# Kernel tuning notes

Hardware: AMD Instinct MI355X
Metric: run time of the kernel (lower is better)

Reference implementation:

```python
import jax, jax.numpy as jnp
import numpy as np

B, T, N, IN, H, K = 8, 10, 50, 6, 256, 4
E = N * (N - 1)


def setup_inputs() -> dict:
    key = jax.random.key(0)
    ks = jax.random.split(key, 22)
    p = lambda k, shape: jax.random.normal(k, shape, jnp.float32) * 0.05
    return {
        "inputs": jax.random.normal(ks[0], (B, T, N, IN), jnp.float32),
        "sampled_edges": jax.random.uniform(ks[1], (B, T, E, K), dtype=jnp.float32),
        "msg_w1": p(ks[2], (K, H, 2 * H)), "msg_b1": p(ks[3], (K, H)),
        "msg_w2": p(ks[4], (K, H, H)), "msg_b2": p(ks[5], (K, H)),
        "w_hr": p(ks[6], (H, H)), "w_hi": p(ks[7], (H, H)), "w_hh": p(ks[8], (H, H)),
        "w_ir": p(ks[9], (H, IN)), "b_ir": p(ks[10], (H,)),
        "w_ii": p(ks[11], (H, IN)), "b_ii": p(ks[12], (H,)),
        "w_in": p(ks[13], (H, IN)), "b_in": p(ks[14], (H,)),
        "w_o1": p(ks[15], (H, H)), "b_o1": p(ks[16], (H,)),
        "w_o2": p(ks[17], (H, H)), "b_o2": p(ks[18], (H,)),
        "w_o3": p(ks[19], (IN, H)), "b_o3": p(ks[20], (IN,)),
    }


def reference(inputs, sampled_edges, msg_w1, msg_b1, msg_w2, msg_b2,
              w_hr, w_hi, w_hh, w_ir, b_ir, w_ii, b_ii, w_in, b_in,
              w_o1, b_o1, w_o2, b_o2, w_o3, b_o3):
    b, t, n, _ = inputs.shape
    k = msg_w1.shape[0]
    h = msg_w1.shape[1]
    # fully-connected directed graph, no self loops (static indices)
    send_np, recv_np = np.where(np.ones((n, n)) - np.eye(n))
    send = jnp.asarray(send_np)
    recv = jnp.asarray(recv_np)
    norm = float(k) - 1.0  # skip_first_edge_type = True

    def single_step(ins, rel, hidden):
        # ins: [B,N,IN], rel: [B,E,K], hidden: [B,N,H]
        pre = jnp.concatenate([hidden[:, recv], hidden[:, send]], axis=-1)  # [B,E,2H]
        all_msgs = jnp.zeros((b, pre.shape[1], h), inputs.dtype)
        for i in range(1, k):  # skip first edge type
            m = jnp.tanh(jnp.einsum('bef,hf->beh', pre, msg_w1[i]) + msg_b1[i])
            m = jnp.tanh(jnp.einsum('beh,jh->bej', m, msg_w2[i]) + msg_b2[i])
            all_msgs = all_msgs + m * rel[:, :, i:i + 1] / norm
        # scatter-add messages to receiver nodes (replaces onehot matmul)
        agg = jnp.zeros((b, n, h), inputs.dtype).at[:, recv].add(all_msgs) / (n - 1)
        r = jax.nn.sigmoid(ins @ w_ir.T + b_ir + agg @ w_hr.T)
        ig = jax.nn.sigmoid(ins @ w_ii.T + b_ii + agg @ w_hi.T)
        nn_ = jnp.tanh(ins @ w_in.T + b_in + r * (agg @ w_hh.T))
        hidden = (1 - ig) * nn_ + ig * hidden
        pred = jax.nn.relu(hidden @ w_o1.T + b_o1)
        pred = jax.nn.relu(pred @ w_o2.T + b_o2)
        pred = ins + (pred @ w_o3.T + b_o3)
        return pred, hidden

    x_t = jnp.swapaxes(inputs, 0, 1)         # [T,B,N,IN]
    e_t = jnp.swapaxes(sampled_edges, 0, 1)  # [T,B,E,K]
    h0 = jnp.zeros((b, n, h), inputs.dtype)

    def step(carry, xs):
        hidden, prev = carry
        xt, et, s = xs
        ins = jnp.where(s == 0, xt, prev)  # teacher_forcing=False: only step 0 uses inputs
        pred, hidden = single_step(ins, et, hidden)
        return (hidden, pred), pred

    _, preds = jax.lax.scan(step, (h0, jnp.zeros_like(x_t[0])), (x_t, e_t, jnp.arange(t)))
    return jnp.swapaxes(preds, 0, 1)  # [B,T,N,IN]
```

## Files before the change

### kernel.cpp

```cpp
#include <hip/hip_runtime.h>
#include <hip/hip_bf16.h>
#include <stdint.h>

#define B_ 8
#define T_ 10
#define N_ 50
#define IN_ 6
#define H_ 256
#define K_ 4
#define E_ 2450
#define ROWS 400
#define AP 102400

typedef __attribute__((ext_vector_type(8))) __bf16 bf16x8;
typedef __attribute__((ext_vector_type(4))) float f32x4;

__device__ __forceinline__ unsigned short f2bf(float x) {
    unsigned int u = __float_as_uint(x);
    u = (u + 0x7fffu + ((u >> 16) & 1u)) >> 16;
    return (unsigned short)u;
}
__device__ __forceinline__ unsigned pk2(float a, float b) {
    return (unsigned)f2bf(a) | ((unsigned)f2bf(b) << 16);
}
__device__ __forceinline__ float rcp_fast(float x) { return __builtin_amdgcn_rcpf(x); }
__device__ __forceinline__ float tanh_fast(float x) {
    float e = __expf(2.0f * x);
    return 1.0f - 2.0f * rcp_fast(e + 1.0f);
}
__device__ __forceinline__ float sigmoid_fast(float x) {
    return rcp_fast(1.0f + __expf(-x));
}

__global__ __launch_bounds__(256) void swizzle_weights(
        const float* __restrict__ w1, const float* __restrict__ w2,
        const float* __restrict__ whr, const float* __restrict__ whi,
        const float* __restrict__ whh, const float* __restrict__ wo1,
        const float* __restrict__ wo2, const float* __restrict__ b1,
        unsigned short* __restrict__ w1s, unsigned short* __restrict__ w2s,
        unsigned short* __restrict__ gws, unsigned short* __restrict__ wos,
        unsigned int* __restrict__ hidden_zero, float* __restrict__ UV) {
    const int W1N = 3 * 16 * 16 * 64 * 8;
    const int W2N = 3 * 16 * 8 * 64 * 8;
    const int GWN = 3 * 65536;
    const int WON = 2 * 65536;
    const int ZN  = 102400;
    int idx = blockIdx.x * 256 + threadIdx.x;
    if (idx < W1N) {
        int j = idx & 7, L = (idx >> 3) & 63, kt = (idx >> 9) & 15;
        int nt = (idx >> 13) & 15, i = idx >> 17;
        int n = nt * 16 + (L & 15);
        int k = kt * 32 + ((L >> 4) << 3) + j;
        w1s[idx] = f2bf(w1[((size_t)(i + 1) * H_ + n) * (2 * H_) + k]);
    } else if (idx < W1N + W2N) {
        int t = idx - W1N;
        int j = t & 7, L = (t >> 3) & 63, kt = (t >> 9) & 7;
        int nt = (t >> 12) & 15, i = t >> 16;
        int n = nt * 16 + (L & 15);
        int k = kt * 32 + ((L >> 4) << 3) + j;
        w2s[t] = f2bf(w2[((size_t)(i + 1) * H_ + n) * H_ + k]);
    } else if (idx < W1N + W2N + GWN) {
        int t = idx - (W1N + W2N);
        int j = t & 7, L = (t >> 3) & 63, kt = (t >> 9) & 7;
        int nt = (t >> 12) & 15, mat = t >> 16;
        int n = nt * 16 + (L & 15);
        int k = kt * 32 + ((L >> 4) << 3) + j;
        const float* src = (mat == 0) ? whr : (mat == 1) ? whi : whh;
        gws[t] = f2bf(src[(size_t)n * H_ + k]);
    } else if (idx < W1N + W2N + GWN + WON) {
        int t = idx - (W1N + W2N + GWN);
        int j = t & 7, L = (t >> 3) & 63, kt = (t >> 9) & 7;
        int nt = (t >> 12) & 15, g = t >> 16;
        int n = nt * 16 + (L & 15);
        int k = kt * 32 + ((L >> 4) << 3) + j;
        const float* src = (g == 0) ? wo1 : wo2;
        wos[t] = f2bf(src[(size_t)n * H_ + k]);
    } else if (idx < W1N + W2N + GWN + WON + ZN) {
        hidden_zero[idx - (W1N + W2N + GWN + WON)] = 0u;
    } else {
        int t = idx - (W1N + W2N + GWN + WON + ZN);
        int c = t & 511;
        int ty = (t >> 9) % 3;
        UV[t] = (c < 256) ? b1[(ty + 1) * H_ + c] : 0.0f;
    }
}

__global__ __launch_bounds__(256, 4) void msgagg_kernel(
        const float* __restrict__ UV, const float* __restrict__ edges,
        const unsigned short* __restrict__ w2s,
        const float* __restrict__ b2, float* __restrict__ aggP, int t) {
    __shared__ unsigned short m1F[32 * 512];
    __shared__ float relS[64];

    int ty = blockIdx.x / 400;
    int rem = blockIdx.x - ty * 400;
    int b = rem / 50;
    int r = rem - b * 50;
    int tid = threadIdx.x;
    int lane = tid & 63, wid = tid >> 6;
    int col = lane & 15, q = lane >> 4;

    if (tid < 64) {
        float v = 0.0f;
        if (tid < 50 && tid != r) {
            int e = tid * 49 + (r > tid ? r - 1 : r);
            v = edges[(((size_t)b * T_ + t) * E_ + e) * K_ + ty + 1];
        }
        relS[tid] = v;
    }

    {
        int row = wid * 16 + col;
        int sv = row < N_ ? row : N_ - 1;
        const float* Vrow = &UV[((size_t)(b * N_ + sv) * 3 + ty) * 512 + 256 + q * 8];
        const float* Urow = &UV[((size_t)(b * N_ + r) * 3 + ty) * 512 + q * 8];
        #pragma unroll
        for (int kt = 0; kt < 8; ++kt) {
            float4 v0 = *(const float4*)(Vrow + kt * 32);
            float4 v1 = *(const float4*)(Vrow + kt * 32 + 4);
            float4 u0 = *(const float4*)(Urow + kt * 32);
            float4 u1 = *(const float4*)(Urow + kt * 32 + 4);
            float m0 = tanh_fast(u0.x + v0.x);
            float m1 = tanh_fast(u0.y + v0.y);
            float m2 = tanh_fast(u0.z + v0.z);
            float m3 = tanh_fast(u0.w + v0.w);
            float m4 = tanh_fast(u1.x + v1.x);
            float m5 = tanh_fast(u1.y + v1.y);
            float m6 = tanh_fast(u1.z + v1.z);
            float m7 = tanh_fast(u1.w + v1.w);
            uint4 pk;
            pk.x = pk2(m0, m1); pk.y = pk2(m2, m3);
            pk.z = pk2(m4, m5); pk.w = pk2(m6, m7);
            *(uint4*)&m1F[(wid * 8 + kt) * 512 + lane * 8] = pk;
        }
    }
    __syncthreads();

    const bf16x8* w2f = (const bf16x8*)w2s;
    f32x4 acc[4][4];
    #pragma unroll
    for (int mt = 0; mt < 4; ++mt)
        #pragma unroll
        for (int u = 0; u < 4; ++u) acc[mt][u] = (f32x4){0.f, 0.f, 0.f, 0.f};

    #pragma unroll
    for (int kt = 0; kt < 8; ++kt) {
        bf16x8 a0 = *(const bf16x8*)&m1F[(0 * 8 + kt) * 512 + lane * 8];
        bf16x8 a1 = *(const bf16x8*)&m1F[(1 * 8 + kt) * 512 + lane * 8];
        bf16x8 a2 = *(const bf16x8*)&m1F[(2 * 8 + kt) * 512 + lane * 8];
        bf16x8 a3 = *(const bf16x8*)&m1F[(3 * 8 + kt) * 512 + lane * 8];
        #pragma unroll
        for (int u = 0; u < 4; ++u) {
            bf16x8 w = w2f[(size_t)((ty * 16 + wid * 4 + u) * 8 + kt) * 64 + lane];
            acc[0][u] = __builtin_amdgcn_mfma_f32_16x16x32_bf16(a0, w, acc[0][u], 0, 0, 0);
            acc[1][u] = __builtin_amdgcn_mfma_f32_16x16x32_bf16(a1, w, acc[1][u], 0, 0, 0);
            acc[2][u] = __builtin_amdgcn_mfma_f32_16x16x32_bf16(a2, w, acc[2][u], 0, 0, 0);
            acc[3][u] = __builtin_amdgcn_mfma_f32_16x16x32_bf16(a3, w, acc[3][u], 0, 0, 0);
        }
    }
    #pragma unroll
    for (int u = 0; u < 4; ++u) {
        float bias = b2[(ty + 1) * H_ + (wid * 4 + u) * 16 + col];
        float sum = 0.0f;
        #pragma unroll
        for (int mt = 0; mt < 4; ++mt)
            #pragma unroll
            for (int rg = 0; rg < 4; ++rg) {
                int row = mt * 16 + q * 4 + rg;
                sum += tanh_fast(acc[mt][u][rg] + bias) * relS[row];
            }
        sum += __shfl_xor(sum, 16);
        sum += __shfl_xor(sum, 32);
        if (lane < 16)
            aggP[(size_t)ty * AP + (size_t)(b * N_ + r) * H_ +
                 (wid * 4 + u) * 16 + col] = sum * (1.0f / 147.0f);
    }
}

__global__ __launch_bounds__(512) void nodeuv_kernel(
        const float* __restrict__ inputs, const float* __restrict__ aggP,
        const unsigned short* __restrict__ gws, const unsigned short* __restrict__ wos,
        const unsigned short* __restrict__ w1s,
        const float* __restrict__ hid_rd, float* __restrict__ hid_wr,
        float* __restrict__ UV,
        const float* __restrict__ w_ir, const float* __restrict__ b_ir,
        const float* __restrict__ w_ii, const float* __restrict__ b_ii,
        const float* __restrict__ w_in, const float* __restrict__ b_in,
        const float* __restrict__ b1,
        const float* __restrict__ b_o1, const float* __restrict__ b_o2,
        const float* __restrict__ w_o3, const float* __restrict__ b_o3,
        float* __restrict__ out, int t) {
    __shared__ unsigned short aggF[8 * 512];
    __shared__ unsigned short hnF[8 * 512];
    __shared__ unsigned short p1F[8 * 512];
    __shared__ float p2L[16 * 260];
    __shared__ float insS[16 * 6];

    int role = blockIdx.x / 25;
    int mm = blockIdx.x - role * 25;
    if (role > 0 && t == T_ - 1) return;

    int tid = threadIdx.x;
    int lane = tid & 63, wid = tid >> 6;
    int col = lane & 15, q = lane >> 4;

    const float* src = (t == 0) ? inputs : out;
    int tt = (t == 0) ? 0 : (t - 1);

    {
        int kt = tid >> 6, L = tid & 63;
        int row = mm * 16 + (L & 15);
        int k0 = kt * 32 + ((L >> 4) << 3);
        const float* p = &aggP[(size_t)row * H_ + k0];
        float4 a0 = *(const float4*)(p);
        float4 a1 = *(const float4*)(p + 4);
        float4 b0 = *(const float4*)(p + AP);
        float4 b1v = *(const float4*)(p + AP + 4);
        float4 c0 = *(const float4*)(p + 2 * AP);
        float4 c1 = *(const float4*)(p + 2 * AP + 4);
        uint4 pk;
        pk.x = pk2(a0.x + b0.x + c0.x, a0.y + b0.y + c0.y);
        pk.y = pk2(a0.z + b0.z + c0.z, a0.w + b0.w + c0.w);
        pk.z = pk2(a1.x + b1v.x + c1.x, a1.y + b1v.y + c1.y);
        pk.w = pk2(a1.z + b1v.z + c1.z, a1.w + b1v.w + c1.w);
        *(uint4*)&aggF[(size_t)kt * 512 + L * 8] = pk;
    }
    if (tid < 96) {
        int rl = tid / 6, c = tid - rl * 6;
        int row = mm * 16 + rl;
        int b = row / 50, n = row - b * 50;
        insS[rl * 6 + c] = src[(((size_t)b * T_ + tt) * N_ + n) * IN_ + c];
    }
    __syncthreads();

    const bf16x8* gwf = (const bf16x8*)gws;
    bf16x8 af[8];
    #pragma unroll
    for (int kt = 0; kt < 8; ++kt)
        af[kt] = *(const bf16x8*)&aggF[kt * 512 + lane * 8];

    f32x4 acc[3][2];
    #pragma unroll
    for (int m = 0; m < 3; ++m)
        #pragma unroll
        for (int u = 0; u < 2; ++u) acc[m][u] = (f32x4){0.f, 0.f, 0.f, 0.f};

    bf16x8 wg[2][2][3][2];
    #pragma unroll
    for (int ki = 0; ki < 2; ++ki)
        #pragma unroll
        for (int m = 0; m < 3; ++m)
            #pragma unroll
            for (int u = 0; u < 2; ++u)
                wg[0][ki][m][u] = gwf[(size_t)((m * 16 + wid * 2 + u) * 8 + ki) * 64 + lane];
    #pragma unroll
    for (int c = 0; c < 4; ++c) {
        if (c < 3) {
            #pragma unroll
            for (int ki = 0; ki < 2; ++ki)
                #pragma unroll
                for (int m = 0; m < 3; ++m)
                    #pragma unroll
                    for (int u = 0; u < 2; ++u)
                        wg[(c + 1) & 1][ki][m][u] =
                            gwf[(size_t)((m * 16 + wid * 2 + u) * 8 + (c + 1) * 2 + ki) * 64 + lane];
        }
        #pragma unroll
        for (int ki = 0; ki < 2; ++ki)
            #pragma unroll
            for (int m = 0; m < 3; ++m)
                #pragma unroll
                for (int u = 0; u < 2; ++u)
                    acc[m][u] = __builtin_amdgcn_mfma_f32_16x16x32_bf16(
                        af[c * 2 + ki], wg[c & 1][ki][m][u], acc[m][u], 0, 0, 0);
    }

    #pragma unroll
    for (int u = 0; u < 2; ++u) {
        int h = (wid * 2 + u) * 16 + col;
        float bir = b_ir[h], bii = b_ii[h], bin_ = b_in[h];
        float wir[6], wii[6], win[6];
        #pragma unroll
        for (int c = 0; c < 6; ++c) {
            wir[c] = w_ir[h * 6 + c];
            wii[c] = w_ii[h * 6 + c];
            win[c] = w_in[h * 6 + c];
        }
        #pragma unroll
        for (int rg = 0; rg < 4; ++rg) {
            int rl = q * 4 + rg;
            int row = mm * 16 + rl;
            float xr = bir, xi = bii, xn = bin_;
            #pragma unroll
            for (int c = 0; c < 6; ++c) {
                float iv = insS[rl * 6 + c];
                xr += wir[c] * iv;
                xi += wii[c] * iv;
                xn += win[c] * iv;
            }
            float rgate = sigmoid_fast(xr + acc[0][u][rg]);
            float igate = sigmoid_fast(xi + acc[1][u][rg]);
            float nn = tanh_fast(xn + rgate * acc[2][u][rg]);
            size_t off = (size_t)row * H_ + h;
            float hold = hid_rd[off];
            float hnew = (1.0f - igate) * nn + igate * hold;
            if (role == 0) hid_wr[off] = hnew;
            hnF[(h >> 5) * 512 + (((h >> 3) & 3) * 16 + rl) * 8 + (h & 7)] = f2bf(hnew);
        }
    }
    __syncthreads();

    if (role > 0) {
        int s = role - 1;
        int ty = s >> 1, half = s & 1;
        const bf16x8* w1f = (const bf16x8*)w1s;
        bf16x8 a2f[8], wv[8][2];
        #pragma unroll
        for (int kt = 0; kt < 8; ++kt) {
            a2f[kt] = *(const bf16x8*)&hnF[kt * 512 + lane * 8];
            #pragma unroll
            for (int u = 0; u < 2; ++u)
                wv[kt][u] = w1f[(size_t)((ty * 16 + wid * 2 + u) * 16 + half * 8 + kt) * 64 + lane];
        }
        f32x4 acc2[2];
        #pragma unroll
        for (int u = 0; u < 2; ++u) acc2[u] = (f32x4){0.f, 0.f, 0.f, 0.f};
        #pragma unroll
        for (int kt = 0; kt < 8; ++kt)
            #pragma unroll
            for (int u = 0; u < 2; ++u)
                acc2[u] = __builtin_amdgcn_mfma_f32_16x16x32_bf16(a2f[kt], wv[kt][u], acc2[u], 0, 0, 0);
        #pragma unroll
        for (int u = 0; u < 2; ++u) {
            int nt = wid * 2 + u;
            float bias = (half == 0) ? b1[(ty + 1) * H_ + nt * 16 + col] : 0.0f;
            #pragma unroll
            for (int r = 0; r < 4; ++r)
                UV[((size_t)(mm * 16 + q * 4 + r) * 3 + ty) * 512 + half * 256 +
                   nt * 16 + col] = acc2[u][r] + bias;
        }
        return;
    }

    const bf16x8* wof = (const bf16x8*)wos;
    {
        bf16x8 a1f[8], w1r[8][2];
        #pragma unroll
        for (int kt = 0; kt < 8; ++kt) {
            a1f[kt] = *(const bf16x8*)&hnF[kt * 512 + lane * 8];
            #pragma unroll
            for (int u = 0; u < 2; ++u)
                w1r[kt][u] = wof[(size_t)((wid * 2 + u) * 8 + kt) * 64 + lane];
        }
        f32x4 a1v[2];
        #pragma unroll
        for (int u = 0; u < 2; ++u) a1v[u] = (f32x4){0.f, 0.f, 0.f, 0.f};
        #pragma unroll
        for (int kt = 0; kt < 8; ++kt)
            #pragma unroll
            for (int u = 0; u < 2; ++u)
                a1v[u] = __builtin_amdgcn_mfma_f32_16x16x32_bf16(a1f[kt], w1r[kt][u], a1v[u], 0, 0, 0);
        #pragma unroll
        for (int u = 0; u < 2; ++u) {
            int h = (wid * 2 + u) * 16 + col;
            float bo = b_o1[h];
            #pragma unroll
            for (int rg = 0; rg < 4; ++rg) {
                int rl = q * 4 + rg;
                float v = fmaxf(a1v[u][rg] + bo, 0.0f);
                p1F[(h >> 5) * 512 + (((h >> 3) & 3) * 16 + rl) * 8 + (h & 7)] = f2bf(v);
            }
        }
    }
    __syncthreads();

    {
        bf16x8 a2f[8], w2r[8][2];
        #pragma unroll
        for (int kt = 0; kt < 8; ++kt) {
            a2f[kt] = *(const bf16x8*)&p1F[kt * 512 + lane * 8];
            #pragma unroll
            for (int u = 0; u < 2; ++u)
                w2r[kt][u] = wof[(size_t)((16 + wid * 2 + u) * 8 + kt) * 64 + lane];
        }
        f32x4 a2v[2];
        #pragma unroll
        for (int u = 0; u < 2; ++u) a2v[u] = (f32x4){0.f, 0.f, 0.f, 0.f};
        #pragma unroll
        for (int kt = 0; kt < 8; ++kt)
            #pragma unroll
            for (int u = 0; u < 2; ++u)
                a2v[u] = __builtin_amdgcn_mfma_f32_16x16x32_bf16(a2f[kt], w2r[kt][u], a2v[u], 0, 0, 0);
        #pragma unroll
        for (int u = 0; u < 2; ++u) {
            int h = (wid * 2 + u) * 16 + col;
            float bo = b_o2[h];
            #pragma unroll
            for (int rg = 0; rg < 4; ++rg) {
                int rl = q * 4 + rg;
                p2L[rl * 260 + h] = fmaxf(a2v[u][rg] + bo, 0.0f);
            }
        }
    }
    __syncthreads();

    if (tid < 192) {
        int o = tid >> 3;
        int part = tid & 7;
        #pragma unroll
        for (int pass = 0; pass < 4; ++pass) {
            int oo = o + pass * 24;
            int rl = oo / 6, c = oo - rl * 6;
            float acc3 = (part == 0) ? b_o3[c] : 0.0f;
            const float* wrow = &w_o3[c * 256];
            const float* prow = &p2L[rl * 260];
            #pragma unroll
            for (int i = 0; i < 8; ++i) {
                int k = i * 32 + part * 4;
                float4 w = *(const float4*)&wrow[k];
                float4 p = *(const float4*)&prow[k];
                acc3 += w.x * p.x + w.y * p.y + w.z * p.z + w.w * p.w;
            }
            acc3 += __shfl_xor(acc3, 1);
            acc3 += __shfl_xor(acc3, 2);
            acc3 += __shfl_xor(acc3, 4);
            if (part == 0) {
                int row = mm * 16 + rl;
                int b = row / 50, n = row - b * 50;
                out[(((size_t)b * T_ + t) * N_ + n) * IN_ + c] = insS[rl * 6 + c] + acc3;
            }
        }
    }
}

extern "C" void kernel_launch(void* const* d_in, const int* in_sizes, int n_in,
                              void* d_out, int out_size, void* d_ws, size_t ws_size,
                              hipStream_t stream) {
    const float* inputs = (const float*)d_in[0];
    const float* edges  = (const float*)d_in[1];
    const float* msg_w1 = (const float*)d_in[2];
    const float* msg_b1 = (const float*)d_in[3];
    const float* msg_w2 = (const float*)d_in[4];
    const float* msg_b2 = (const float*)d_in[5];
    const float* w_hr = (const float*)d_in[6];
    const float* w_hi = (const float*)d_in[7];
    const float* w_hh = (const float*)d_in[8];
    const float* w_ir = (const float*)d_in[9];
    const float* b_ir = (const float*)d_in[10];
    const float* w_ii = (const float*)d_in[11];
    const float* b_ii = (const float*)d_in[12];
    const float* w_in = (const float*)d_in[13];
    const float* b_in = (const float*)d_in[14];
    const float* w_o1 = (const float*)d_in[15];
    const float* b_o1 = (const float*)d_in[16];
    const float* w_o2 = (const float*)d_in[17];
    const float* b_o2 = (const float*)d_in[18];
    const float* w_o3 = (const float*)d_in[19];
    const float* b_o3 = (const float*)d_in[20];
    float* out = (float*)d_out;

    char* ws = (char*)d_ws;
    float* hidden0           = (float*)(ws);
    float* hidden1           = (float*)(ws + 409600);
    float* UV                = (float*)(ws + 819200);
    float* aggP              = (float*)(ws + 3276800);
    unsigned short* w1s      = (unsigned short*)(ws + 4505600);
    unsigned short* w2s      = (unsigned short*)(ws + 5292032);
    unsigned short* gws      = (unsigned short*)(ws + 5685248);
    unsigned short* wos      = (unsigned short*)(ws + 6078464);

    swizzle_weights<<<dim3(6384), dim3(256), 0, stream>>>(
        msg_w1, msg_w2, w_hr, w_hi, w_hh, w_o1, w_o2, msg_b1,
        w1s, w2s, gws, wos, (unsigned int*)hidden0, UV);

    float* hid[2] = {hidden0, hidden1};
    for (int t = 0; t < T_; ++t) {
        msgagg_kernel<<<dim3(1200), dim3(256), 0, stream>>>(
            UV, edges, w2s, msg_b2, aggP, t);
        nodeuv_kernel<<<dim3(175), dim3(512), 0, stream>>>(
            inputs, aggP, gws, wos, w1s, hid[t & 1], hid[(t + 1) & 1], UV,
            w_ir, b_ir, w_ii, b_ii, w_in, b_in, msg_b1,
            b_o1, b_o2, w_o3, b_o3, out, t);
    }
}
```

Baseline: 494.1 us.

## Merge UV halves per block and prefetch post-GRU weights before gate epilogue

The node kernel now uses 4 roles per row tile instead of 7: each message-type role computes both halves of the UV projection, so the grid drops from 175 to 100 blocks. The first post-GRU weight tile (w_o1 or the first half of msg_w1) is loaded into registers before the GRU gate epilogue, hiding global-load latency behind that math. The w_o2 weights are also loaded before the first output MLP matmul. A launch_bounds occupancy hint of 2 blocks is added. In exchange, each block does more serial MFMA work and register pressure rises, which could cause spills under the 2-block bound.

```diff
diff --git a/kernel.cpp b/kernel.cpp
--- a/kernel.cpp
+++ b/kernel.cpp
@@ -177,7 +177,7 @@
     }
 }
 
-__global__ __launch_bounds__(512) void nodeuv_kernel(
+__global__ __launch_bounds__(512, 2) void nodeuv_kernel(
         const float* __restrict__ inputs, const float* __restrict__ aggP,
         const unsigned short* __restrict__ gws, const unsigned short* __restrict__ wos,
         const unsigned short* __restrict__ w1s,
@@ -275,6 +275,24 @@
                         af[c * 2 + ki], wg[c & 1][ki][m][u], acc[m][u], 0, 0, 0);
     }
 
+    const bf16x8* wof = (const bf16x8*)wos;
+    const bf16x8* w1f = (const bf16x8*)w1s;
+    bf16x8 tw[8][2];
+    if (role == 0) {
+        #pragma unroll
+        for (int kt = 0; kt < 8; ++kt)
+            #pragma unroll
+            for (int u = 0; u < 2; ++u)
+                tw[kt][u] = wof[(size_t)((wid * 2 + u) * 8 + kt) * 64 + lane];
+    } else {
+        int ty = role - 1;
+        #pragma unroll
+        for (int kt = 0; kt < 8; ++kt)
+            #pragma unroll
+            for (int u = 0; u < 2; ++u)
+                tw[kt][u] = w1f[(size_t)((ty * 16 + wid * 2 + u) * 16 + kt) * 64 + lane];
+    }
+
     #pragma unroll
     for (int u = 0; u < 2; ++u) {
         int h = (wid * 2 + u) * 16 + col;
@@ -311,47 +329,58 @@
     __syncthreads();
 
     if (role > 0) {
-        int s = role - 1;
-        int ty = s >> 1, half = s & 1;
-        const bf16x8* w1f = (const bf16x8*)w1s;
-        bf16x8 a2f[8], wv[8][2];
-        #pragma unroll
-        for (int kt = 0; kt < 8; ++kt) {
+        int ty = role - 1;
+        bf16x8 a2f[8];
+        #pragma unroll
+        for (int kt = 0; kt < 8; ++kt)
             a2f[kt] = *(const bf16x8*)&hnF[kt * 512 + lane * 8];
-            #pragma unroll
-            for (int u = 0; u < 2; ++u)
-                wv[kt][u] = w1f[(size_t)((ty * 16 + wid * 2 + u) * 16 + half * 8 + kt) * 64 + lane];
-        }
-        f32x4 acc2[2];
-        #pragma unroll
-        for (int u = 0; u < 2; ++u) acc2[u] = (f32x4){0.f, 0.f, 0.f, 0.f};
-        #pragma unroll
-        for (int kt = 0; kt < 8; ++kt)
-            #pragma unroll
-            for (int u = 0; u < 2; ++u)
-                acc2[u] = __builtin_amdgcn_mfma_f32_16x16x32_bf16(a2f[kt], wv[kt][u], acc2[u], 0, 0, 0);
+        bf16x8 wv1[8][2];
+        #pragma unroll
+        for (int kt = 0; kt < 8; ++kt)
+            #pragma unroll
+            for (int u = 0; u < 2; ++u)
+                wv1[kt][u] = w1f[(size_t)((ty * 16 + wid * 2 + u) * 16 + 8 + kt) * 64 + lane];
+        f32x4 acc0[2], acc1[2];
+        #pragma unroll
+        for (int u = 0; u < 2; ++u) {
+            acc0[u] = (f32x4){0.f, 0.f, 0.f, 0.f};
+            acc1[u] = (f32x4){0.f, 0.f, 0.f, 0.f};
+        }
+        #pragma unroll
+        for (int kt = 0; kt < 8; ++kt)
+            #pragma unroll
+            for (int u = 0; u < 2; ++u)
+                acc0[u] = __builtin_amdgcn_mfma_f32_16x16x32_bf16(a2f[kt], tw[kt][u], acc0[u], 0, 0, 0);
+        #pragma unroll
+        for (int kt = 0; kt < 8; ++kt)
+            #pragma unroll
+            for (int u = 0; u < 2; ++u)
+                acc1[u] = __builtin_amdgcn_mfma_f32_16x16x32_bf16(a2f[kt], wv1[kt][u], acc1[u], 0, 0, 0);
         #pragma unroll
         for (int u = 0; u < 2; ++u) {
             int nt = wid * 2 + u;
-            float bias = (half == 0) ? b1[(ty + 1) * H_ + nt * 16 + col] : 0.0f;
-            #pragma unroll
-            for (int r = 0; r < 4; ++r)
-                UV[((size_t)(mm * 16 + q * 4 + r) * 3 + ty) * 512 + half * 256 +
-                   nt * 16 + col] = acc2[u][r] + bias;
+            float bias = b1[(ty + 1) * H_ + nt * 16 + col];
+            #pragma unroll
+            for (int r = 0; r < 4; ++r) {
+                size_t base = ((size_t)(mm * 16 + q * 4 + r) * 3 + ty) * 512 + nt * 16 + col;
+                UV[base] = acc0[u][r] + bias;
+                UV[base + 256] = acc1[u][r];
+            }
         }
         return;
     }
 
-    const bf16x8* wof = (const bf16x8*)wos;
     {
-        bf16x8 a1f[8], w1r[8][2];
-        #pragma unroll
-        for (int kt = 0; kt < 8; ++kt) {
+        bf16x8 a1f[8];
+        #pragma unroll
+        for (int kt = 0; kt < 8; ++kt)
             a1f[kt] = *(const bf16x8*)&hnF[kt * 512 + lane * 8];
-            #pragma unroll
-            for (int u = 0; u < 2; ++u)
-                w1r[kt][u] = wof[(size_t)((wid * 2 + u) * 8 + kt) * 64 + lane];
-        }
+        bf16x8 o2w[8][2];
+        #pragma unroll
+        for (int kt = 0; kt < 8; ++kt)
+            #pragma unroll
+            for (int u = 0; u < 2; ++u)
+                o2w[kt][u] = wof[(size_t)((16 + wid * 2 + u) * 8 + kt) * 64 + lane];
         f32x4 a1v[2];
         #pragma unroll
         for (int u = 0; u < 2; ++u) a1v[u] = (f32x4){0.f, 0.f, 0.f, 0.f};
@@ -359,7 +388,7 @@
         for (int kt = 0; kt < 8; ++kt)
             #pragma unroll
             for (int u = 0; u < 2; ++u)
-                a1v[u] = __builtin_amdgcn_mfma_f32_16x16x32_bf16(a1f[kt], w1r[kt][u], a1v[u], 0, 0, 0);
+                a1v[u] = __builtin_amdgcn_mfma_f32_16x16x32_bf16(a1f[kt], tw[kt][u], a1v[u], 0, 0, 0);
         #pragma unroll
         for (int u = 0; u < 2; ++u) {
             int h = (wid * 2 + u) * 16 + col;
@@ -371,18 +400,12 @@
                 p1F[(h >> 5) * 512 + (((h >> 3) & 3) * 16 + rl) * 8 + (h & 7)] = f2bf(v);
             }
         }
-    }
-    __syncthreads();
-
-    {
-        bf16x8 a2f[8], w2r[8][2];
-        #pragma unroll
-        for (int kt = 0; kt < 8; ++kt) {
+        __syncthreads();
+
+        bf16x8 a2f[8];
+        #pragma unroll
+        for (int kt = 0; kt < 8; ++kt)
             a2f[kt] = *(const bf16x8*)&p1F[kt * 512 + lane * 8];
-            #pragma unroll
-            for (int u = 0; u < 2; ++u)
-                w2r[kt][u] = wof[(size_t)((16 + wid * 2 + u) * 8 + kt) * 64 + lane];
-        }
         f32x4 a2v[2];
         #pragma unroll
         for (int u = 0; u < 2; ++u) a2v[u] = (f32x4){0.f, 0.f, 0.f, 0.f};
@@ -390,7 +413,7 @@
         for (int kt = 0; kt < 8; ++kt)
             #pragma unroll
             for (int u = 0; u < 2; ++u)
-                a2v[u] = __builtin_amdgcn_mfma_f32_16x16x32_bf16(a2f[kt], w2r[kt][u], a2v[u], 0, 0, 0);
+                a2v[u] = __builtin_amdgcn_mfma_f32_16x16x32_bf16(a2f[kt], o2w[kt][u], a2v[u], 0, 0, 0);
         #pragma unroll
         for (int u = 0; u < 2; ++u) {
             int h = (wid * 2 + u) * 16 + col;
@@ -477,7 +500,7 @@
     for (int t = 0; t < T_; ++t) {
         msgagg_kernel<<<dim3(1200), dim3(256), 0, stream>>>(
             UV, edges, w2s, msg_b2, aggP, t);
-        nodeuv_kernel<<<dim3(175), dim3(512), 0, stream>>>(
+        nodeuv_kernel<<<dim3(100), dim3(512), 0, stream>>>(
             inputs, aggP, gws, wos, w1s, hid[t & 1], hid[(t + 1) & 1], UV,
             w_ir, b_ir, w_ii, b_ii, w_in, b_in, msg_b1,
             b_o1, b_o2, w_o3, b_o3, out, t);
```

New measurement: 499.0 us. No clear change (+1.0%).
